# Optimization experiments

Measured on AMD Instinct MI355X. Metric: run time of the kernel, lower is better.

Reference implementation:

```python
import jax, jax.numpy as jnp
import numpy as np

N, L, E, H = 8, 1024, 512, 4


def setup_inputs() -> dict:
    key = jax.random.key(0)
    ks = jax.random.split(key, 10)
    s = 1.0 / np.sqrt(E)
    return {
        "modalA": jax.random.normal(ks[0], (N, L, E), dtype=jnp.float32),
        "modalB": jax.random.normal(ks[1], (N, L, E), dtype=jnp.float32),
        "WqA": jax.random.normal(ks[2], (E, E), dtype=jnp.float32) * s,
        "bqA": jax.random.normal(ks[3], (E,), dtype=jnp.float32) * s,
        "WkA": jax.random.normal(ks[4], (E, E), dtype=jnp.float32) * s,
        "bkA": jax.random.normal(ks[5], (E,), dtype=jnp.float32) * s,
        "WqB": jax.random.normal(ks[6], (E, E), dtype=jnp.float32) * s,
        "bqB": jax.random.normal(ks[7], (E,), dtype=jnp.float32) * s,
        "WkB": jax.random.normal(ks[8], (E, E), dtype=jnp.float32) * s,
        "bkB": jax.random.normal(ks[9], (E,), dtype=jnp.float32) * s,
    }


def reference(modalA, modalB, WqA, bqA, WkA, bkA, WqB, bqB, WkB, bkB):
    # torch Linear: y = x @ W.T + b
    qA = modalA @ WqA.T + bqA  # [N, L, E]
    kA = modalA @ WkA.T + bkA
    qB = modalB @ WqB.T + bqB
    kB = modalB @ WkB.T + bkB

    # mean over heads of per-head dot products == full-dim dot / num_heads
    # (algebraically identical to einsum('nqhd,nkhd->nhqk').mean(1))
    inv_scale = 1.0 / (H * np.sqrt(E).astype(np.float32))

    def attn(q, k):
        scores = jnp.einsum('nqd,nkd->nqk', q, k) * inv_scale  # [N, L, L]
        return jax.nn.softmax(scores, axis=-1)

    weighted_A = attn(qA, kA)
    weighted_B = attn(qB, kB)
    weighted_AB = attn(qA, kB)
    weighted_BA = attn(qB, kA)

    cat_lower = jnp.concatenate([weighted_A, weighted_AB], axis=-1)  # [N, L, 2L]
    cat_upper = jnp.concatenate([weighted_B, weighted_BA], axis=-1)  # [N, L, 2L]
    cat = jnp.concatenate([cat_lower, cat_upper], axis=1)            # [N, 2L, 2L]
    return jnp.mean(cat, axis=0)                                     # [2L, 2L]
```

## Files before the change

### kernel.cpp

```cpp
#include <hip/hip_runtime.h>
#include <hip/hip_bf16.h>

typedef __bf16 bf16;
typedef bf16 bf16x8 __attribute__((ext_vector_type(8)));
typedef _Float16 f16;
typedef f16 f16x8 __attribute__((ext_vector_type(8)));
typedef float f32x4 __attribute__((ext_vector_type(4)));

constexpr int LL = 1024;
constexpr int EE = 512;
constexpr int NBATCH = 8;

__device__ __forceinline__ f32x4 mfma16(bf16x8 a, bf16x8 b, f32x4 c) {
    return __builtin_amdgcn_mfma_f32_16x16x32_bf16(a, b, c, 0, 0, 0);
}

#define GLOAD_LDS16(g, l)                                                     \
    __builtin_amdgcn_global_load_lds(                                         \
        (const __attribute__((address_space(1))) void*)(g),                   \
        (__attribute__((address_space(3))) void*)(l), 16, 0, 0)

constexpr int WAIT_VM6_LG0 = 0x076;
constexpr int WAIT_VM0_LG0 = 0x070;

template <int IMM>
__device__ __forceinline__ void pipe_barrier() {
    __asm__ volatile("" ::: "memory");
    __builtin_amdgcn_s_waitcnt(IMM);
    __builtin_amdgcn_sched_barrier(0);
    __builtin_amdgcn_s_barrier();
    __builtin_amdgcn_sched_barrier(0);
    __asm__ volatile("" ::: "memory");
}

struct CvtParams {
    const float* src[4];
    bf16* dst[4];
    int n8[4];
};

__global__ __launch_bounds__(256) void cvt_kernel(CvtParams p) {
    const int y = blockIdx.y;
    const float* __restrict__ src = p.src[y];
    bf16* __restrict__ dst = p.dst[y];
    const int n8 = p.n8[y];
    for (int i = blockIdx.x * 256 + threadIdx.x; i < n8; i += gridDim.x * 256) {
        float4 a = *(const float4*)(src + (size_t)i * 8);
        float4 b = *(const float4*)(src + (size_t)i * 8 + 4);
        bf16x8 o;
        o[0] = (bf16)a.x; o[1] = (bf16)a.y; o[2] = (bf16)a.z; o[3] = (bf16)a.w;
        o[4] = (bf16)b.x; o[5] = (bf16)b.y; o[6] = (bf16)b.z; o[7] = (bf16)b.w;
        *(bf16x8*)(dst + (size_t)i * 8) = o;
    }
}

struct ProjParams {
    const float* x[4];
    const bf16* w[4];
    const float* b[4];
};

__global__ __launch_bounds__(256, 2) void proj_kernel(ProjParams p, bf16* __restrict__ outbase) {
    const int f = blockIdx.x;
    const int xcd = f & 7;
    const int u = f >> 3;
    const int mz = xcd >> 2;
    const int by = (xcd & 3) * 16 + (u & 15);
    const int zq = (u >> 4) & 1;
    const int bxp = u >> 5;
    const int z = mz * 2 + zq;

    const float* __restrict__ X = p.x[z];
    const bf16* __restrict__ W = p.w[z];
    const float* __restrict__ Bv = p.b[z];
    bf16* __restrict__ O = outbase + (size_t)z * (NBATCH * LL) * EE;

    __shared__ union {
        struct {
            alignas(16) float Af[2][128][32];
            alignas(16) bf16  Bs[2][256][32];
        } st;
        alignas(16) bf16 ep[64][264];
    } sm;

    const int t = threadIdx.x;
    const int lane = t & 63, wid = t >> 6;
    const int wm = wid & 1, wn = wid >> 1;
    const int lr = lane & 15, kg = lane >> 4;

    f32x4 acc[4][8] = {};

    const int ar = t >> 3;
    const int ac = t & 7;
    const int sA = (ar >> 1) & 7;
    const int agc = (ac ^ sA) * 4;
    const float* Xrow0 = X + (size_t)(by * 128 + ar) * EE + agc;

    const int srow = t >> 2;
    const int cgl = t & 3;
    const int gcg = (cgl ^ ((srow >> 1) & 3)) * 8;
    const int scg = (kg ^ ((lr >> 1) & 3)) * 8;
    const bf16* Wrow0 = W + (size_t)(bxp * 256 + srow) * EE + gcg;

    const int cgLo = (2 * kg) ^ ((lr >> 1) & 7);
    const int cgHi = cgLo ^ 1;

    auto stage = [&](int k, int b) {
        const int k0 = k * 32;
#pragma unroll
        for (int i = 0; i < 4; ++i)
            GLOAD_LDS16(Xrow0 + (size_t)(32 * i) * EE + k0, &sm.st.Af[b][32 * i + ar][ac * 4]);
#pragma unroll
        for (int i = 0; i < 4; ++i)
            GLOAD_LDS16(Wrow0 + (size_t)(64 * i) * EE + k0, &sm.st.Bs[b][srow + 64 * i][cgl * 8]);
    };
    auto compute = [&](int b) {
        bf16x8 af[4], bfr[8];
#pragma unroll
        for (int im = 0; im < 4; ++im) {
            const int row = wm * 64 + im * 16 + lr;
            f32x4 lo = *(const f32x4*)&sm.st.Af[b][row][cgLo * 4];
            f32x4 hi = *(const f32x4*)&sm.st.Af[b][row][cgHi * 4];
#pragma unroll
            for (int e = 0; e < 4; ++e) {
                af[im][e] = (bf16)lo[e];
                af[im][4 + e] = (bf16)hi[e];
            }
        }
#pragma unroll
        for (int in = 0; in < 8; ++in)
            bfr[in] = *(const bf16x8*)&sm.st.Bs[b][wn * 128 + in * 16 + lr][scg];
#pragma unroll
        for (int im = 0; im < 4; ++im)
#pragma unroll
            for (int in = 0; in < 8; ++in)
                acc[im][in] = mfma16(af[im], bfr[in], acc[im][in]);
    };

    stage(0, 0);
#pragma unroll
    for (int k = 0; k < 16; ++k) {
        pipe_barrier<WAIT_VM0_LG0>();
        if (k < 15) stage(k + 1, (k + 1) & 1);
        compute(k & 1);
    }
    __syncthreads();

#pragma unroll
    for (int pph = 0; pph < 2; ++pph) {
        if (wm == pph) {
#pragma unroll
            for (int im = 0; im < 4; ++im) {
                const int row = im * 16 + kg * 4;
#pragma unroll
                for (int in = 0; in < 8; ++in) {
                    const int col = wn * 128 + in * 16 + lr;
                    const float bias = Bv[bxp * 256 + col];
#pragma unroll
                    for (int r = 0; r < 4; ++r)
                        sm.ep[row + r][col] = (bf16)(acc[im][in][r] + bias);
                }
            }
        }
        __syncthreads();
#pragma unroll
        for (int i = 0; i < 8; ++i) {
            const int c = i * 256 + t;
            const int row = c >> 5, colg = (c & 31) * 8;
            *(uint4*)(O + (size_t)(by * 128 + pph * 64 + row) * EE + bxp * 256 + colg) =
                *(const uint4*)&sm.ep[row][colg];
        }
        __syncthreads();
    }
}

struct ScoresParams {
    const bf16* q[4];
    const bf16* k[4];
    f16* s[4];
};

__global__ __launch_bounds__(256, 2) void scores_kernel(ScoresParams p) {
    const int f = blockIdx.x;
    const int xcd = f & 7;
    const int j = f >> 3;
    const int z = (xcd << 2) + (j >> 5);
    const int map = z >> 3, n = z & 7;
    const int tile = j & 31;
    const int bxp = tile & 3, by = tile >> 2;

    const bf16* __restrict__ Qb = p.q[map] + (size_t)n * LL * EE;
    const bf16* __restrict__ Kb = p.k[map] + (size_t)n * LL * EE;
    f16* __restrict__ Sb = p.s[map] + (size_t)n * LL * LL;

    __shared__ union {
        struct { alignas(16) bf16 A[3][128][32]; alignas(16) bf16 B[3][256][32]; } st;
        alignas(16) f16 ep[64][264];
    } sm;

    const int t = threadIdx.x;
    const int lane = t & 63, wid = t >> 6;
    const int wm = wid & 1, wn = wid >> 1;
    const int lr = lane & 15, kg = lane >> 4;

    f32x4 acc[4][8] = {};

    const int srow = t >> 2;
    const int cgl = t & 3;
    const int gcg = (cgl ^ ((srow >> 1) & 3)) * 8;
    const int scg = (kg ^ ((lr >> 1) & 3)) * 8;

    const bf16* Qrow0 = Qb + (size_t)(by * 128 + srow) * EE + gcg;
    const bf16* Krow0 = Kb + (size_t)(bxp * 256 + srow) * EE + gcg;

    auto stage = [&](int k, int b) {
        const int k0 = k * 32;
#pragma unroll
        for (int i = 0; i < 2; ++i)
            GLOAD_LDS16(Qrow0 + (size_t)(64 * i) * EE + k0, &sm.st.A[b][srow + 64 * i][cgl * 8]);
#pragma unroll
        for (int i = 0; i < 4; ++i)
            GLOAD_LDS16(Krow0 + (size_t)(64 * i) * EE + k0, &sm.st.B[b][srow + 64 * i][cgl * 8]);
    };
    auto compute = [&](int b) {
        bf16x8 af[4], bfr[8];
#pragma unroll
        for (int im = 0; im < 4; ++im)
            af[im] = *(const bf16x8*)&sm.st.A[b][wm * 64 + im * 16 + lr][scg];
#pragma unroll
        for (int in = 0; in < 8; ++in)
            bfr[in] = *(const bf16x8*)&sm.st.B[b][wn * 128 + in * 16 + lr][scg];
#pragma unroll
        for (int im = 0; im < 4; ++im)
#pragma unroll
            for (int in = 0; in < 8; ++in)
                acc[im][in] = mfma16(af[im], bfr[in], acc[im][in]);
    };

    stage(0, 0);
    stage(1, 1);
#pragma unroll
    for (int k = 0; k < 16; ++k) {
        if (k < 15) pipe_barrier<WAIT_VM6_LG0>();
        else        pipe_barrier<WAIT_VM0_LG0>();
        if (k < 14) stage(k + 2, (k + 2) % 3);
        compute(k % 3);
    }
    __syncthreads();

    const float inv_scale = 0.011048543456039806f;
#pragma unroll
    for (int pph = 0; pph < 2; ++pph) {
        if (wm == pph) {
#pragma unroll
            for (int im = 0; im < 4; ++im) {
                const int row = im * 16 + kg * 4;
#pragma unroll
                for (int in = 0; in < 8; ++in) {
                    const int col = wn * 128 + in * 16 + lr;
#pragma unroll
                    for (int r = 0; r < 4; ++r)
                        sm.ep[row + r][col] = (f16)(acc[im][in][r] * inv_scale);
                }
            }
        }
        __syncthreads();
#pragma unroll
        for (int i = 0; i < 8; ++i) {
            const int c = i * 256 + t;
            const int row = c >> 5, colg = (c & 31) * 8;
            *(uint4*)(Sb + (size_t)(by * 128 + pph * 64 + row) * LL + bxp * 256 + colg) =
                *(const uint4*)&sm.ep[row][colg];
        }
        __syncthreads();
    }
}

struct SmParams {
    const f16* s[4];
};

__global__ __launch_bounds__(256) void softmax_mean_kernel(SmParams p, float* __restrict__ out) {
    const int map = blockIdx.y;
    const f16* __restrict__ S = p.s[map];
    const int t = threadIdx.x;
    const int half = t >> 7;
    const int tl = t & 127;
    const int q = blockIdx.x * 2 + half;
    const int lane = t & 63, wid = t >> 6;
    __shared__ float red[NBATCH][4];

    f16x8 v[NBATCH];
#pragma unroll
    for (int n = 0; n < NBATCH; ++n)
        v[n] = *(const f16x8*)(S + ((size_t)n * LL + q) * LL + tl * 8);

    float e[NBATCH][8];
#pragma unroll
    for (int n = 0; n < NBATCH; ++n) {
        float s = 0.f;
#pragma unroll
        for (int j = 0; j < 8; ++j) {
            e[n][j] = __expf((float)v[n][j]);
            s += e[n][j];
        }
#pragma unroll
        for (int off = 32; off; off >>= 1) s += __shfl_xor(s, off);
        if (lane == 0) red[n][wid] = s;
    }
    __syncthreads();

    float acc[8] = {};
#pragma unroll
    for (int n = 0; n < NBATCH; ++n) {
        const float inv = 0.125f / (red[n][half * 2] + red[n][half * 2 + 1]);
#pragma unroll
        for (int j = 0; j < 8; ++j) acc[j] += e[n][j] * inv;
    }

    const int orow = (map >= 2 ? LL : 0) + q;
    const int ocol = (map & 1 ? LL : 0) + tl * 8;
    float* o = out + (size_t)orow * (2 * LL) + ocol;
    *(float4*)(o + 0) = make_float4(acc[0], acc[1], acc[2], acc[3]);
    *(float4*)(o + 4) = make_float4(acc[4], acc[5], acc[6], acc[7]);
}

extern "C" void kernel_launch(void* const* d_in, const int* in_sizes, int n_in,
                              void* d_out, int out_size, void* d_ws, size_t ws_size,
                              hipStream_t stream) {
    const float* modalA = (const float*)d_in[0];
    const float* modalB = (const float*)d_in[1];
    const float* WqA = (const float*)d_in[2];
    const float* bqA = (const float*)d_in[3];
    const float* WkA = (const float*)d_in[4];
    const float* bkA = (const float*)d_in[5];
    const float* WqB = (const float*)d_in[6];
    const float* bqB = (const float*)d_in[7];
    const float* WkB = (const float*)d_in[8];
    const float* bkB = (const float*)d_in[9];
    float* out = (float*)d_out;

    const size_t projN = (size_t)(NBATCH * LL) * EE;
    const size_t mapN = (size_t)NBATCH * LL * LL;
    char* base = (char*)d_ws;
    bf16* qk = (bf16*)base;
    char* region2 = base + 4 * projN * sizeof(bf16);
    bf16* W4 = (bf16*)region2;
    f16* S = (f16*)region2;

    CvtParams cp;
    const float* wsrc[4] = {WqA, WkA, WqB, WkB};
    for (int i = 0; i < 4; ++i) {
        cp.src[i] = wsrc[i];
        cp.dst[i] = W4 + (size_t)i * EE * EE;
        cp.n8[i] = EE * EE / 8;
    }
    cvt_kernel<<<dim3(128, 4), 256, 0, stream>>>(cp);

    ProjParams pp;
    pp.x[0] = modalA; pp.x[1] = modalA; pp.x[2] = modalB; pp.x[3] = modalB;
    for (int i = 0; i < 4; ++i) pp.w[i] = W4 + (size_t)i * EE * EE;
    pp.b[0] = bqA; pp.b[1] = bkA; pp.b[2] = bqB; pp.b[3] = bkB;
    proj_kernel<<<dim3(512), 256, 0, stream>>>(pp, qk);

    const bf16* qA = qk + 0 * projN;
    const bf16* kA = qk + 1 * projN;
    const bf16* qB = qk + 2 * projN;
    const bf16* kB = qk + 3 * projN;

    ScoresParams sp;
    sp.q[0] = qA; sp.q[1] = qA; sp.q[2] = qB; sp.q[3] = qB;
    sp.k[0] = kA; sp.k[1] = kB; sp.k[2] = kB; sp.k[3] = kA;
    for (int m = 0; m < 4; ++m) sp.s[m] = S + (size_t)m * mapN;
    scores_kernel<<<dim3(1024), 256, 0, stream>>>(sp);

    SmParams smp;
    for (int m = 0; m < 4; ++m) smp.s[m] = S + (size_t)m * mapN;
    softmax_mean_kernel<<<dim3(512, 4), 256, 0, stream>>>(smp, out);
}
```

Before: 171.9 us.

## Fuse exp and row-sum partials into scores epilogue, simplify softmax-mean pass

The scores kernel now writes exp(scaled score) in fp16 and computes per-tile row partial sums, stored in a global buffer. The softmax-mean kernel then only scales the exp values by the reciprocal of the summed partials, with no block reduction or sync. The scores launch is also split into two half launches by map. This removes the per-row reduction from the memory-bound pass but adds exp and shuffle work to the GEMM epilogue, an extra launch, and no max subtraction.

```diff
diff --git a/kernel.cpp b/kernel.cpp
--- a/kernel.cpp
+++ b/kernel.cpp
@@ -10,6 +10,8 @@
 constexpr int LL = 1024;
 constexpr int EE = 512;
 constexpr int NBATCH = 8;
+
+__device__ float g_sums[4 * NBATCH * LL * 4];
 
 __device__ __forceinline__ f32x4 mfma16(bf16x8 a, bf16x8 b, f32x4 c) {
     return __builtin_amdgcn_mfma_f32_16x16x32_bf16(a, b, c, 0, 0, 0);
@@ -178,14 +180,16 @@
     const bf16* q[4];
     const bf16* k[4];
     f16* s[4];
+    int mapbase;
 };
 
 __global__ __launch_bounds__(256, 2) void scores_kernel(ScoresParams p) {
     const int f = blockIdx.x;
     const int xcd = f & 7;
     const int j = f >> 3;
-    const int z = (xcd << 2) + (j >> 5);
-    const int map = z >> 3, n = z & 7;
+    const int z2 = (xcd << 1) + (j >> 5);
+    const int map = p.mapbase + (z2 >> 3);
+    const int n = z2 & 7;
     const int tile = j & 31;
     const int bxp = tile & 3, by = tile >> 2;
 
@@ -195,7 +199,7 @@
 
     __shared__ union {
         struct { alignas(16) bf16 A[3][128][32]; alignas(16) bf16 B[3][256][32]; } st;
-        alignas(16) f16 ep[64][264];
+        struct { alignas(16) f16 ep[64][264]; float rs[128][2]; } ew;
     } sm;
 
     const int t = threadIdx.x;
@@ -255,12 +259,25 @@
 #pragma unroll
             for (int im = 0; im < 4; ++im) {
                 const int row = im * 16 + kg * 4;
+                float rsl[4] = {0.f, 0.f, 0.f, 0.f};
 #pragma unroll
                 for (int in = 0; in < 8; ++in) {
                     const int col = wn * 128 + in * 16 + lr;
 #pragma unroll
-                    for (int r = 0; r < 4; ++r)
-                        sm.ep[row + r][col] = (f16)(acc[im][in][r] * inv_scale);
+                    for (int r = 0; r < 4; ++r) {
+                        const float ev = __expf(acc[im][in][r] * inv_scale);
+                        sm.ew.ep[row + r][col] = (f16)ev;
+                        rsl[r] += ev;
+                    }
+                }
+#pragma unroll
+                for (int r = 0; r < 4; ++r) {
+                    float v = rsl[r];
+                    v += __shfl_xor(v, 1);
+                    v += __shfl_xor(v, 2);
+                    v += __shfl_xor(v, 4);
+                    v += __shfl_xor(v, 8);
+                    if (lr == 0) sm.ew.rs[pph * 64 + row + r][wn] = v;
                 }
             }
         }
@@ -270,9 +287,14 @@
             const int c = i * 256 + t;
             const int row = c >> 5, colg = (c & 31) * 8;
             *(uint4*)(Sb + (size_t)(by * 128 + pph * 64 + row) * LL + bxp * 256 + colg) =
-                *(const uint4*)&sm.ep[row][colg];
+                *(const uint4*)&sm.ew.ep[row][colg];
         }
         __syncthreads();
+    }
+
+    if (t < 128) {
+        const float d = sm.ew.rs[t][0] + sm.ew.rs[t][1];
+        g_sums[(((size_t)(map * NBATCH + n) * LL) + by * 128 + t) * 4 + bxp] = d;
     }
 }
 
@@ -282,40 +304,20 @@
 
 __global__ __launch_bounds__(256) void softmax_mean_kernel(SmParams p, float* __restrict__ out) {
     const int map = blockIdx.y;
-    const f16* __restrict__ S = p.s[map];
+    const f16* __restrict__ E = p.s[map];
     const int t = threadIdx.x;
     const int half = t >> 7;
     const int tl = t & 127;
     const int q = blockIdx.x * 2 + half;
-    const int lane = t & 63, wid = t >> 6;
-    __shared__ float red[NBATCH][4];
-
-    f16x8 v[NBATCH];
-#pragma unroll
-    for (int n = 0; n < NBATCH; ++n)
-        v[n] = *(const f16x8*)(S + ((size_t)n * LL + q) * LL + tl * 8);
-
-    float e[NBATCH][8];
+
+    float acc[8] = {};
 #pragma unroll
     for (int n = 0; n < NBATCH; ++n) {
-        float s = 0.f;
-#pragma unroll
-        for (int j = 0; j < 8; ++j) {
-            e[n][j] = __expf((float)v[n][j]);
-            s += e[n][j];
-        }
-#pragma unroll
-        for (int off = 32; off; off >>= 1) s += __shfl_xor(s, off);
-        if (lane == 0) red[n][wid] = s;
-    }
-    __syncthreads();
-
-    float acc[8] = {};
-#pragma unroll
-    for (int n = 0; n < NBATCH; ++n) {
-        const float inv = 0.125f / (red[n][half * 2] + red[n][half * 2 + 1]);
-#pragma unroll
-        for (int j = 0; j < 8; ++j) acc[j] += e[n][j] * inv;
+        f16x8 v = *(const f16x8*)(E + ((size_t)n * LL + q) * LL + tl * 8);
+        const float4 s4 = *(const float4*)&g_sums[(((size_t)(map * NBATCH + n) * LL) + q) * 4];
+        const float w = 0.125f / (s4.x + s4.y + s4.z + s4.w);
+#pragma unroll
+        for (int jj = 0; jj < 8; ++jj) acc[jj] += (float)v[jj] * w;
     }
 
     const int orow = (map >= 2 ? LL : 0) + q;
@@ -372,7 +374,10 @@
     sp.q[0] = qA; sp.q[1] = qA; sp.q[2] = qB; sp.q[3] = qB;
     sp.k[0] = kA; sp.k[1] = kB; sp.k[2] = kB; sp.k[3] = kA;
     for (int m = 0; m < 4; ++m) sp.s[m] = S + (size_t)m * mapN;
-    scores_kernel<<<dim3(1024), 256, 0, stream>>>(sp);
+    sp.mapbase = 0;
+    scores_kernel<<<dim3(512), 256, 0, stream>>>(sp);
+    sp.mapbase = 2;
+    scores_kernel<<<dim3(512), 256, 0, stream>>>(sp);
 
     SmParams smp;
     for (int m = 0; m < 4; ++m) smp.s[m] = S + (size_t)m * mapN;
```

After: 190.7 us. 1.11x slower.
